# Optimization experiments

Hardware: AMD Instinct MI355X
Metric: run time of the kernel (lower is better)

Reference implementation:

```python
import jax, jax.numpy as jnp
import numpy as np

N_NODES = 100000
N_EDGES = 1600000
IN_DIM = 256
OUT_DIM = 128
SELF_LOOP_W = 2.0  # improved=True


def setup_inputs() -> dict:
    key = jax.random.key(0)
    ks = jax.random.split(key, 9)
    x = jax.random.normal(ks[0], (N_NODES, IN_DIM), dtype=jnp.float32)
    edge_index = jax.random.randint(ks[1], (2, N_EDGES), 0, N_NODES, dtype=jnp.int64)
    edge_weight = jax.random.uniform(ks[2], (N_EDGES,), dtype=jnp.float32)
    s1 = 1.0 / np.sqrt(IN_DIM)
    s2 = 1.0 / np.sqrt(OUT_DIM)
    W1 = jax.random.normal(ks[3], (IN_DIM, OUT_DIM), dtype=jnp.float32) * s1
    b1 = jnp.zeros((OUT_DIM,), dtype=jnp.float32)
    W_mu = jax.random.normal(ks[4], (OUT_DIM, OUT_DIM), dtype=jnp.float32) * s2
    b_mu = jnp.zeros((OUT_DIM,), dtype=jnp.float32)
    W_var = jax.random.normal(ks[5], (OUT_DIM, OUT_DIM), dtype=jnp.float32) * s2
    b_var = jnp.zeros((OUT_DIM,), dtype=jnp.float32)
    return {"x": x, "edge_index": edge_index, "edge_weight": edge_weight,
            "W1": W1, "b1": b1, "W_mu": W_mu, "b_mu": b_mu,
            "W_var": W_var, "b_var": b_var}


def _gcn_norm(edge_index, edge_weight, num_nodes):
    # add self loops with fill value 2.0 (improved=True), then symmetric norm
    loop = jnp.arange(num_nodes, dtype=edge_index.dtype)
    row = jnp.concatenate([edge_index[0], loop])
    col = jnp.concatenate([edge_index[1], loop])
    ew = jnp.concatenate([edge_weight,
                          jnp.full((num_nodes,), SELF_LOOP_W, dtype=edge_weight.dtype)])
    deg = jax.ops.segment_sum(ew, col, num_segments=num_nodes)
    dis = jnp.where(deg > 0, jax.lax.rsqrt(jnp.where(deg > 0, deg, 1.0)), 0.0)
    norm = dis[row] * ew * dis[col]
    return row, col, norm


def _gcn_conv(x, row, col, norm, W, b, num_nodes):
    xw = x @ W                      # [N, out]
    msg = xw[row] * norm[:, None]   # [E+N, out] per-edge messages
    out = jax.ops.segment_sum(msg, col, num_segments=num_nodes)
    return out + b


def reference(x, edge_index, edge_weight, W1, b1, W_mu, b_mu, W_var, b_var):
    n = x.shape[0]
    row, col, norm = _gcn_norm(edge_index, edge_weight, n)
    feat = jax.nn.relu(_gcn_conv(x, row, col, norm, W1, b1, n))
    mu = _gcn_conv(feat, row, col, norm, W_mu, b_mu, n)
    var = _gcn_conv(feat, row, col, norm, W_var, b_var, n)
    return (mu, var)
```

## Files before the change

### kernel.cpp

```cpp
#include <hip/hip_runtime.h>
#include <hip/hip_bf16.h>

#define CDIV(a,b) (((a)+(b)-1)/(b))

typedef __attribute__((ext_vector_type(8))) short short8;
typedef __attribute__((ext_vector_type(4))) float f32x4;

static __device__ inline short f2bf(float f) {
    union { __hip_bfloat16 h; short s; } u;
    u.h = __float2bfloat16(f);
    return u.s;
}
static __device__ inline ushort f2bfu(float f) { return (ushort)f2bf(f); }
static __device__ inline float bfu_lo(uint v) { return __uint_as_float(v << 16); }
static __device__ inline float bfu_hi(uint v) { return __uint_as_float(v & 0xffff0000u); }


__global__ __launch_bounds__(512) void k_init(unsigned long long* __restrict__ pack, int n,
                                              const float* __restrict__ W1,
                                              short* __restrict__ W1t,
                                              const float* __restrict__ Wmu,
                                              const float* __restrict__ Wvar,
                                              short* __restrict__ Wcat) {
    int i = blockIdx.x * 512 + threadIdx.x;
    if (i < n) pack[i] = 0ull;
    if (i < 128 * 256) {
        int k = i % 256, col = i / 256;
        W1t[i] = f2bf(W1[(size_t)k * 128 + col]);
    } else if (i < 2 * 128 * 256) {
        int j = i - 128 * 256;
        int k = j & 127, col = j >> 7;
        float v = (col < 128) ? Wmu[(size_t)k * 128 + col] : Wvar[(size_t)k * 128 + (col - 128)];
        Wcat[j] = f2bf(v);
    }
}


__global__ __launch_bounds__(512) void k_fat(const float* __restrict__ A,
                                             const short* __restrict__ Bt,
                                             ushort* __restrict__ C, int n, int nGB,
                                             const int* __restrict__ col,
                                             const float* __restrict__ ew,
                                             unsigned long long* __restrict__ pack,
                                             int* __restrict__ rank, int E) {
    const int K = 256, KH = 128;
    __shared__ short Blds[128 * KH];
    int t = threadIdx.x;

    if (blockIdx.x >= nGB) {
        int e = (blockIdx.x - nGB) * 512 + t;
        if (e < E) {
            int c = col[e];
            unsigned long long q = (unsigned long long)(ew[e] * 16777216.0f + 0.5f);
            unsigned long long old = atomicAdd(&pack[c], (1ull << 40) | q);
            rank[e] = (int)(old >> 40);
        }
        return;
    }

    int wave = t >> 6, lane = t & 63;
    int lg = lane >> 4, lr = lane & 15;
    long row_base = (long)blockIdx.x * 256 + wave * 32;

    long ra0 = row_base + lr;      if (ra0 > n - 1) ra0 = n - 1;
    long ra1 = row_base + 16 + lr; if (ra1 > n - 1) ra1 = n - 1;

    f32x4 acc[2][8];
    #pragma unroll
    for (int i = 0; i < 2; ++i)
        #pragma unroll
        for (int j = 0; j < 8; ++j) acc[i][j] = (f32x4){0.f, 0.f, 0.f, 0.f};

    const float* pa0 = A + ra0 * K + lg * 8;
    const float* pa1 = A + ra1 * K + lg * 8;

    #pragma unroll
    for (int p = 0; p < 2; ++p) {
        if (p) __syncthreads();
        const int CHK = KH / 8;
        for (int c = t; c < 128 * CHK; c += 512) {
            int colw = c / CHK;
            int kb  = (c % CHK) * 16;
            int dst = colw * (KH * 2) + (kb ^ ((colw & 7) << 4));
            *(float4*)((char*)Blds + dst) =
                *(const float4*)((const char*)Bt + (size_t)colw * (K * 2) + p * (KH * 2) + kb);
        }
        __syncthreads();

        for (int k0 = 0; k0 < KH; k0 += 32) {
            int kg = p * KH + k0;
            float4 x0 = *(const float4*)(pa0 + kg);
            float4 x1 = *(const float4*)(pa0 + kg + 4);
            float4 y0 = *(const float4*)(pa1 + kg);
            float4 y1 = *(const float4*)(pa1 + kg + 4);
            short8 a0, a1;
            a0[0]=f2bf(x0.x); a0[1]=f2bf(x0.y); a0[2]=f2bf(x0.z); a0[3]=f2bf(x0.w);
            a0[4]=f2bf(x1.x); a0[5]=f2bf(x1.y); a0[6]=f2bf(x1.z); a0[7]=f2bf(x1.w);
            a1[0]=f2bf(y0.x); a1[1]=f2bf(y0.y); a1[2]=f2bf(y0.z); a1[3]=f2bf(y0.w);
            a1[4]=f2bf(y1.x); a1[5]=f2bf(y1.y); a1[6]=f2bf(y1.z); a1[7]=f2bf(y1.w);

            int kb = (k0 + lg * 8) * 2;
            #pragma unroll
            for (int cb = 0; cb < 8; ++cb) {
                int colm = cb * 16 + lr;
                short8 b = *(short8*)((char*)Blds + colm * (KH * 2) + (kb ^ ((colm & 7) << 4)));
                acc[0][cb] = __builtin_amdgcn_mfma_f32_16x16x32_bf16(a0, b, acc[0][cb], 0, 0, 0);
                acc[1][cb] = __builtin_amdgcn_mfma_f32_16x16x32_bf16(a1, b, acc[1][cb], 0, 0, 0);
            }
        }
    }

    #pragma unroll
    for (int rf = 0; rf < 2; ++rf) {
        #pragma unroll
        for (int cb = 0; cb < 8; ++cb) {
            int colm = cb * 16 + lr;
            #pragma unroll
            for (int r = 0; r < 4; ++r) {
                long row = row_base + rf * 16 + lg * 4 + r;
                if (row < n) C[row * 128 + colm] = f2bfu(acc[rf][cb][r]);
            }
        }
    }
}


__global__ __launch_bounds__(256) void k_scan1(const unsigned long long* __restrict__ pack,
                                               float* __restrict__ dis,
                                               int* __restrict__ row_ptr,
                                               int* __restrict__ bsum, int n) {
    int t = threadIdx.x;
    int base = blockIdx.x * 1024 + t * 4;
    int v0 = 0, v1 = 0, v2 = 0, v3 = 0;
    #pragma unroll
    for (int j = 0; j < 4; ++j) {
        int idx = base + j;
        if (idx < n) {
            unsigned long long p = pack[idx];
            float deg = 2.0f + (float)(p & ((1ull << 40) - 1)) * (1.0f / 16777216.0f);
            dis[idx] = rsqrtf(deg);
            int c = (int)(p >> 40);
            if (j == 0) v0 = c; else if (j == 1) v1 = c; else if (j == 2) v2 = c; else v3 = c;
        }
    }
    int tsum = v0 + v1 + v2 + v3;
    int lane = t & 63, wv = t >> 6;
    int val = tsum;
    #pragma unroll
    for (int d = 1; d < 64; d <<= 1) {
        int u = __shfl_up(val, d, 64);
        if (lane >= d) val += u;
    }
    __shared__ int ws[4];
    if (lane == 63) ws[wv] = val;
    __syncthreads();
    int woff = 0;
    #pragma unroll
    for (int i = 0; i < 4; ++i) if (i < wv) woff += ws[i];
    int excl = woff + val - tsum;
    if (base + 0 < n) row_ptr[base + 0] = excl;  excl += v0;
    if (base + 1 < n) row_ptr[base + 1] = excl;  excl += v1;
    if (base + 2 < n) row_ptr[base + 2] = excl;  excl += v2;
    if (base + 3 < n) row_ptr[base + 3] = excl;
    if (t == 255) bsum[blockIdx.x] = woff + val;
}

__global__ __launch_bounds__(128) void k_scan2(int* bsum, int nb, int* row_ptr, int n, int E) {
    int t = threadIdx.x;
    int v = (t < nb) ? bsum[t] : 0;
    int lane = t & 63, wv = t >> 6;
    int val = v;
    #pragma unroll
    for (int d = 1; d < 64; d <<= 1) {
        int u = __shfl_up(val, d, 64);
        if (lane >= d) val += u;
    }
    __shared__ int ws[2];
    if (lane == 63) ws[wv] = val;
    __syncthreads();
    int woff = (wv == 1) ? ws[0] : 0;
    if (t < nb) bsum[t] = woff + val - v;
    if (t == 0) row_ptr[n] = E;
}

__global__ __launch_bounds__(256) void k_scan3(int* __restrict__ row_ptr,
                                               const int* __restrict__ bsum, int n) {
    int i = blockIdx.x * 256 + threadIdx.x;
    if (i < n) row_ptr[i] += bsum[i >> 10];
}

__global__ __launch_bounds__(512) void k_fill(const int* __restrict__ rowi,
                                              const int* __restrict__ coli,
                                              const float* __restrict__ ew,
                                              const int* __restrict__ rank,
                                              const float* __restrict__ dis,
                                              const int* __restrict__ row_ptr,
                                              int2* __restrict__ csr, int E) {
    int e = blockIdx.x * 512 + threadIdx.x;
    if (e < E) {
        int c = coli[e], r = rowi[e];
        int pos = row_ptr[c] + rank[e];
        csr[pos] = make_int2(r, __float_as_int(dis[r] * ew[e]));
    }
}


template<int OUTMODE>
__global__ __launch_bounds__(256) void k_agg(const uint2* __restrict__ src,
                                             const int* __restrict__ row_ptr,
                                             const int2* __restrict__ csr,
                                             const float* __restrict__ dis,
                                             const float* __restrict__ bias,
                                             uint2* __restrict__ dst, int n) {
    int wid = (blockIdx.x * 256 + threadIdx.x) >> 6;
    int lane = threadIdx.x & 63;
    int hb = lane >> 5, lc = lane & 31;
    if (wid >= n) return;
    int e0 = row_ptr[wid], e1 = row_ptr[wid + 1];

    float p00=0.f,p01=0.f,p02=0.f,p03=0.f;
    float p10=0.f,p11=0.f,p12=0.f,p13=0.f;
    float p20=0.f,p21=0.f,p22=0.f,p23=0.f;
    float p30=0.f,p31=0.f,p32=0.f,p33=0.f;

    int e = e0;
    for (; e + 7 < e1; e += 8) {
        int2 c0 = csr[e     + hb];
        int2 c1 = csr[e + 2 + hb];
        int2 c2 = csr[e + 4 + hb];
        int2 c3 = csr[e + 6 + hb];
        uint2 v0 = src[(size_t)c0.x * 32 + lc];
        uint2 v1 = src[(size_t)c1.x * 32 + lc];
        uint2 v2 = src[(size_t)c2.x * 32 + lc];
        uint2 v3 = src[(size_t)c3.x * 32 + lc];
        float w0 = __int_as_float(c0.y), w1 = __int_as_float(c1.y);
        float w2 = __int_as_float(c2.y), w3 = __int_as_float(c3.y);
        p00 += w0 * bfu_lo(v0.x); p01 += w0 * bfu_hi(v0.x);
        p02 += w0 * bfu_lo(v0.y); p03 += w0 * bfu_hi(v0.y);
        p10 += w1 * bfu_lo(v1.x); p11 += w1 * bfu_hi(v1.x);
        p12 += w1 * bfu_lo(v1.y); p13 += w1 * bfu_hi(v1.y);
        p20 += w2 * bfu_lo(v2.x); p21 += w2 * bfu_hi(v2.x);
        p22 += w2 * bfu_lo(v2.y); p23 += w2 * bfu_hi(v2.y);
        p30 += w3 * bfu_lo(v3.x); p31 += w3 * bfu_hi(v3.x);
        p32 += w3 * bfu_lo(v3.y); p33 += w3 * bfu_hi(v3.y);
    }
    for (; e + 1 < e1; e += 2) {
        int2 c = csr[e + hb];
        uint2 v = src[(size_t)c.x * 32 + lc];
        float w = __int_as_float(c.y);
        p00 += w * bfu_lo(v.x); p01 += w * bfu_hi(v.x);
        p02 += w * bfu_lo(v.y); p03 += w * bfu_hi(v.y);
    }
    if (e < e1 && hb == 0) {
        int2 c = csr[e];
        uint2 v = src[(size_t)c.x * 32 + lc];
        float w = __int_as_float(c.y);
        p10 += w * bfu_lo(v.x); p11 += w * bfu_hi(v.x);
        p12 += w * bfu_lo(v.y); p13 += w * bfu_hi(v.y);
    }

    float x0 = (p00 + p10) + (p20 + p30);
    float x1 = (p01 + p11) + (p21 + p31);
    float x2 = (p02 + p12) + (p22 + p32);
    float x3 = (p03 + p13) + (p23 + p33);
    x0 = x0 + __shfl_xor(x0, 32);
    x1 = x1 + __shfl_xor(x1, 32);
    x2 = x2 + __shfl_xor(x2, 32);
    x3 = x3 + __shfl_xor(x3, 32);

    float dc = dis[wid];
    uint2 sv = src[(size_t)wid * 32 + lc];
    float sw = 2.f * dc * dc;
    float o0 = dc * x0 + sw * bfu_lo(sv.x);
    float o1 = dc * x1 + sw * bfu_hi(sv.x);
    float o2 = dc * x2 + sw * bfu_lo(sv.y);
    float o3 = dc * x3 + sw * bfu_hi(sv.y);
    if constexpr (OUTMODE == 0) {
        float4 bv = *(const float4*)(bias + lc * 4);
        o0 += bv.x; o1 += bv.y; o2 += bv.z; o3 += bv.w;
        o0 = fmaxf(o0, 0.f); o1 = fmaxf(o1, 0.f);
        o2 = fmaxf(o2, 0.f); o3 = fmaxf(o3, 0.f);
    }
    if (hb == 0)
        dst[(size_t)wid * 32 + lc] =
            make_uint2((uint)f2bfu(o0) | ((uint)f2bfu(o1) << 16),
                       (uint)f2bfu(o2) | ((uint)f2bfu(o3) << 16));
}


__global__ __launch_bounds__(512) void k_gemm2(const short* __restrict__ A,
                                               const short* __restrict__ Bt,
                                               const float* __restrict__ bmu,
                                               const float* __restrict__ bvar,
                                               float* __restrict__ out,
                                               int n) {
    const int K = 128;
    __shared__ short Blds[256 * K];
    int t = threadIdx.x;

    const int CHK = K / 8;
    for (int c = t; c < 256 * CHK; c += 512) {
        int col = c / CHK;
        int kb  = (c % CHK) * 16;
        int dst = col * (K * 2) + (kb ^ ((col & 7) << 4));
        *(float4*)((char*)Blds + dst) =
            *(const float4*)((const char*)Bt + (size_t)col * (K * 2) + kb);
    }
    __syncthreads();

    int wave = t >> 6, lane = t & 63;
    int lg = lane >> 4, lr = lane & 15;
    int colbase = (wave & 1) * 128;
    long row_base = (long)blockIdx.x * 128 + (wave >> 1) * 32;

    long ra0 = row_base + lr;      if (ra0 > n - 1) ra0 = n - 1;
    long ra1 = row_base + 16 + lr; if (ra1 > n - 1) ra1 = n - 1;

    f32x4 acc[2][8];
    #pragma unroll
    for (int i = 0; i < 2; ++i)
        #pragma unroll
        for (int j = 0; j < 8; ++j) acc[i][j] = (f32x4){0.f, 0.f, 0.f, 0.f};

    const short* pa0 = A + ra0 * K + lg * 8;
    const short* pa1 = A + ra1 * K + lg * 8;

    #pragma unroll
    for (int k0 = 0; k0 < K; k0 += 32) {
        short8 a0 = *(const short8*)(pa0 + k0);
        short8 a1 = *(const short8*)(pa1 + k0);
        int kb = (k0 + lg * 8) * 2;
        #pragma unroll
        for (int cb = 0; cb < 8; ++cb) {
            int col = colbase + cb * 16 + lr;
            short8 b = *(short8*)((char*)Blds + col * (K * 2) + (kb ^ ((col & 7) << 4)));
            acc[0][cb] = __builtin_amdgcn_mfma_f32_16x16x32_bf16(a0, b, acc[0][cb], 0, 0, 0);
            acc[1][cb] = __builtin_amdgcn_mfma_f32_16x16x32_bf16(a1, b, acc[1][cb], 0, 0, 0);
        }
    }

    #pragma unroll
    for (int rf = 0; rf < 2; ++rf) {
        #pragma unroll
        for (int cb = 0; cb < 8; ++cb) {
            int colc = colbase + cb * 16 + lr;
            bool is_var = colc >= 128;
            int col = is_var ? colc - 128 : colc;
            float bv = is_var ? bvar[col] : bmu[col];
            size_t obase = is_var ? (size_t)n * 128 : 0;
            #pragma unroll
            for (int r = 0; r < 4; ++r) {
                long row = row_base + rf * 16 + lg * 4 + r;
                if (row < n)
                    __builtin_nontemporal_store(acc[rf][cb][r] + bv,
                                                &out[obase + (size_t)row * 128 + col]);
            }
        }
    }
}


extern "C" void kernel_launch(void* const* d_in, const int* in_sizes, int n_in,
                              void* d_out, int out_size, void* d_ws, size_t ws_size,
                              hipStream_t stream) {
    const float* x    = (const float*)d_in[0];
    const int*   ei   = (const int*)d_in[1];
    const float* ew   = (const float*)d_in[2];
    const float* W1   = (const float*)d_in[3];
    const float* b1   = (const float*)d_in[4];
    const float* Wmu  = (const float*)d_in[5];
    const float* bmu  = (const float*)d_in[6];
    const float* Wvar = (const float*)d_in[7];
    const float* bvar = (const float*)d_in[8];

    const int E = in_sizes[2];
    const int N = in_sizes[0] / 256;
    const int* rowi = ei;
    const int* coli = ei + E;

    char* base = (char*)d_ws;
    size_t off = 0;
    auto alloc = [&](size_t bytes) -> void* {
        void* p = base + off;
        off = (off + bytes + 511) & ~(size_t)511;
        return p;
    };
    unsigned long long* pack = (unsigned long long*)alloc((size_t)N * 8);
    float* dis     = (float*)alloc((size_t)N * 4);
    int*   row_ptr = (int*)  alloc((size_t)(N + 1) * 4);
    int*   rank    = (int*)  alloc((size_t)E * 4);
    int*   bsum    = (int*)  alloc(1024 * 4);
    int2*  csr     = (int2*) alloc((size_t)E * 8);
    uint*  xw      = (uint*) alloc((size_t)N * 64 * 4);
    uint*  feat    = (uint*) alloc((size_t)N * 64 * 4);
    short* W1t     = (short*)alloc((size_t)256 * 128 * 2);
    short* Wcat    = (short*)alloc((size_t)256 * 128 * 2);
    uint*  g       = xw;

    int nb   = CDIV(N, 1024);
    int nGB  = CDIV(N, 256);
    int nCB  = CDIV(E, 512);

    k_init<<<CDIV(N, 512), 512, 0, stream>>>(pack, N, W1, W1t, Wmu, Wvar, Wcat);

    k_fat<<<nGB + nCB, 512, 0, stream>>>(x, W1t, (ushort*)xw, N, nGB, coli, ew, pack, rank, E);

    k_scan1<<<nb, 256, 0, stream>>>(pack, dis, row_ptr, bsum, N);
    k_scan2<<<1, 128, 0, stream>>>(bsum, nb, row_ptr, N, E);
    k_scan3<<<CDIV(N, 256), 256, 0, stream>>>(row_ptr, bsum, N);
    k_fill <<<CDIV(E, 512), 512, 0, stream>>>(rowi, coli, ew, rank, dis, row_ptr, csr, E);

    k_agg<0><<<CDIV(N * 64, 256), 256, 0, stream>>>((const uint2*)xw, row_ptr, csr, dis, b1, (uint2*)feat, N);
    k_agg<1><<<CDIV(N * 64, 256), 256, 0, stream>>>((const uint2*)feat, row_ptr, csr, dis, nullptr, (uint2*)g, N);
    k_gemm2<<<CDIV(N, 128), 512, 0, stream>>>((const short*)g, Wcat, bmu, bvar, (float*)d_out, N);
}
```

Measured before the change: 307.1 us.

## Build CSR via two-level bucketed counting sort instead of global atomics

Replaces the global 64-bit atomicAdd degree/rank counting, which was fused into the GEMM launch, with a two-pass bucket sort. Edges are first histogrammed and scattered into 512-node buckets, then ranked and their weights summed with LDS atomics, and finally placed into the CSR. This is meant to remove contended global atomics and the random scatter. In exchange it adds many more kernel launches and extra passes over the edge arrays, and it no longer overlaps edge work with the first GEMM.

```diff
diff --git a/kernel.cpp b/kernel.cpp
--- a/kernel.cpp
+++ b/kernel.cpp
@@ -16,14 +16,12 @@
 static __device__ inline float bfu_hi(uint v) { return __uint_as_float(v & 0xffff0000u); }
 
 
-__global__ __launch_bounds__(512) void k_init(unsigned long long* __restrict__ pack, int n,
-                                              const float* __restrict__ W1,
+__global__ __launch_bounds__(512) void k_init(const float* __restrict__ W1,
                                               short* __restrict__ W1t,
                                               const float* __restrict__ Wmu,
                                               const float* __restrict__ Wvar,
                                               short* __restrict__ Wcat) {
     int i = blockIdx.x * 512 + threadIdx.x;
-    if (i < n) pack[i] = 0ull;
     if (i < 128 * 256) {
         int k = i % 256, col = i / 256;
         W1t[i] = f2bf(W1[(size_t)k * 128 + col]);
@@ -36,27 +34,150 @@
 }
 
 
-__global__ __launch_bounds__(512) void k_fat(const float* __restrict__ A,
-                                             const short* __restrict__ Bt,
-                                             ushort* __restrict__ C, int n, int nGB,
-                                             const int* __restrict__ col,
-                                             const float* __restrict__ ew,
-                                             unsigned long long* __restrict__ pack,
-                                             int* __restrict__ rank, int E) {
+__global__ __launch_bounds__(512) void k_bhist(const int* __restrict__ coli,
+                                               int* __restrict__ bhist,
+                                               int E, int chunk, int nbk) {
+    __shared__ int h[256];
+    int b = blockIdx.x, t = threadIdx.x, nblk = gridDim.x;
+    for (int i = t; i < nbk; i += 512) h[i] = 0;
+    __syncthreads();
+    int e0 = b * chunk, e1 = min(E, e0 + chunk);
+    for (int e = e0 + t; e < e1; e += 512)
+        atomicAdd(&h[coli[e] >> 9], 1);
+    __syncthreads();
+    for (int i = t; i < nbk; i += 512)
+        bhist[i * nblk + b] = h[i];
+}
+
+__global__ __launch_bounds__(256) void kscanA(const int* __restrict__ in,
+                                              int* __restrict__ out,
+                                              int* __restrict__ part, int n) {
+    int t = threadIdx.x;
+    int base = blockIdx.x * 1024 + t * 4;
+    int v0 = (base + 0 < n) ? in[base + 0] : 0;
+    int v1 = (base + 1 < n) ? in[base + 1] : 0;
+    int v2 = (base + 2 < n) ? in[base + 2] : 0;
+    int v3 = (base + 3 < n) ? in[base + 3] : 0;
+    int tsum = v0 + v1 + v2 + v3;
+    int lane = t & 63, wv = t >> 6;
+    int val = tsum;
+    #pragma unroll
+    for (int d = 1; d < 64; d <<= 1) {
+        int u = __shfl_up(val, d, 64);
+        if (lane >= d) val += u;
+    }
+    __shared__ int ws[4];
+    if (lane == 63) ws[wv] = val;
+    __syncthreads();
+    int woff = 0;
+    #pragma unroll
+    for (int i = 0; i < 4; ++i) if (i < wv) woff += ws[i];
+    int excl = woff + val - tsum;
+    if (base + 0 < n) out[base + 0] = excl;  excl += v0;
+    if (base + 1 < n) out[base + 1] = excl;  excl += v1;
+    if (base + 2 < n) out[base + 2] = excl;  excl += v2;
+    if (base + 3 < n) out[base + 3] = excl;
+    if (t == 255) part[blockIdx.x] = woff + val;
+}
+
+__global__ __launch_bounds__(128) void kscanB(int* part, int nb, int* tailp, int tailv) {
+    int t = threadIdx.x;
+    int v = (t < nb) ? part[t] : 0;
+    int lane = t & 63, wv = t >> 6;
+    int val = v;
+    #pragma unroll
+    for (int d = 1; d < 64; d <<= 1) {
+        int u = __shfl_up(val, d, 64);
+        if (lane >= d) val += u;
+    }
+    __shared__ int ws[2];
+    if (lane == 63) ws[wv] = val;
+    __syncthreads();
+    int woff = (wv == 1) ? ws[0] : 0;
+    if (t < nb) part[t] = woff + val - v;
+    if (t == 0 && tailp) *tailp = tailv;
+}
+
+__global__ __launch_bounds__(256) void kscanC(int* __restrict__ out,
+                                              const int* __restrict__ part, int n) {
+    int i = blockIdx.x * 256 + threadIdx.x;
+    if (i < n) out[i] += part[i >> 10];
+}
+
+__global__ __launch_bounds__(512) void k_bucket(const int* __restrict__ rowi,
+                                                const int* __restrict__ coli,
+                                                const float* __restrict__ ew,
+                                                const int* __restrict__ excl,
+                                                int* __restrict__ bcol,
+                                                int2* __restrict__ bre,
+                                                int E, int chunk, int nbk) {
+    __shared__ int cur[256];
+    int b = blockIdx.x, t = threadIdx.x, nblk = gridDim.x;
+    for (int i = t; i < nbk; i += 512) cur[i] = 0;
+    __syncthreads();
+    int e0 = b * chunk, e1 = min(E, e0 + chunk);
+    for (int e = e0 + t; e < e1; e += 512) {
+        int c = coli[e];
+        int bk = c >> 9;
+        int pos = excl[bk * nblk + b] + atomicAdd(&cur[bk], 1);
+        bcol[pos] = c;
+        bre[pos]  = make_int2(rowi[e], __float_as_int(ew[e]));
+    }
+}
+
+__global__ __launch_bounds__(512) void k_fine(const int* __restrict__ bcol,
+                                              const int2* __restrict__ bre,
+                                              const int* __restrict__ excl,
+                                              int* __restrict__ rank,
+                                              int* __restrict__ gcnt,
+                                              int* __restrict__ gews,
+                                              int E, int nblk, int n) {
+    __shared__ int cnt[512], ews[512];
+    int bk = blockIdx.x, t = threadIdx.x;
+    cnt[t] = 0; ews[t] = 0;
+    __syncthreads();
+    int s0 = excl[bk * nblk];
+    int s1 = (bk + 1 < gridDim.x) ? excl[(bk + 1) * nblk] : E;
+    for (int p = s0 + t; p < s1; p += 512) {
+        int cl = bcol[p] & 511;
+        rank[p] = atomicAdd(&cnt[cl], 1);
+        int q = (int)(__int_as_float(bre[p].y) * 16777216.0f + 0.5f);
+        atomicAdd(&ews[cl], q);
+    }
+    __syncthreads();
+    int c = bk * 512 + t;
+    if (c < n) { gcnt[c] = cnt[t]; gews[c] = ews[t]; }
+}
+
+__global__ __launch_bounds__(256) void k_dis(const int* __restrict__ gews,
+                                             float* __restrict__ dis, int n) {
+    int i = blockIdx.x * 256 + threadIdx.x;
+    if (i < n)
+        dis[i] = rsqrtf(2.0f + (float)gews[i] * (1.0f / 16777216.0f));
+}
+
+__global__ __launch_bounds__(512) void k_place(const int* __restrict__ bcol,
+                                               const int2* __restrict__ bre,
+                                               const int* __restrict__ rank,
+                                               const int* __restrict__ row_ptr,
+                                               const float* __restrict__ dis,
+                                               int2* __restrict__ csr, int E) {
+    int p = blockIdx.x * 512 + threadIdx.x;
+    if (p < E) {
+        int c = bcol[p];
+        int2 re = bre[p];
+        csr[row_ptr[c] + rank[p]] =
+            make_int2(re.x, __float_as_int(dis[re.x] * __int_as_float(re.y)));
+    }
+}
+
+
+__global__ __launch_bounds__(512) void k_gemm1(const float* __restrict__ A,
+                                               const short* __restrict__ Bt,
+                                               ushort* __restrict__ C, int n) {
     const int K = 256, KH = 128;
     __shared__ short Blds[128 * KH];
     int t = threadIdx.x;
-
-    if (blockIdx.x >= nGB) {
-        int e = (blockIdx.x - nGB) * 512 + t;
-        if (e < E) {
-            int c = col[e];
-            unsigned long long q = (unsigned long long)(ew[e] * 16777216.0f + 0.5f);
-            unsigned long long old = atomicAdd(&pack[c], (1ull << 40) | q);
-            rank[e] = (int)(old >> 40);
-        }
-        return;
-    }
 
     int wave = t >> 6, lane = t & 63;
     int lg = lane >> 4, lr = lane & 15;
@@ -103,9 +224,9 @@
             #pragma unroll
             for (int cb = 0; cb < 8; ++cb) {
                 int colm = cb * 16 + lr;
-                short8 b = *(short8*)((char*)Blds + colm * (KH * 2) + (kb ^ ((colm & 7) << 4)));
-                acc[0][cb] = __builtin_amdgcn_mfma_f32_16x16x32_bf16(a0, b, acc[0][cb], 0, 0, 0);
-                acc[1][cb] = __builtin_amdgcn_mfma_f32_16x16x32_bf16(a1, b, acc[1][cb], 0, 0, 0);
+                short8 bfr = *(short8*)((char*)Blds + colm * (KH * 2) + (kb ^ ((colm & 7) << 4)));
+                acc[0][cb] = __builtin_amdgcn_mfma_f32_16x16x32_bf16(a0, bfr, acc[0][cb], 0, 0, 0);
+                acc[1][cb] = __builtin_amdgcn_mfma_f32_16x16x32_bf16(a1, bfr, acc[1][cb], 0, 0, 0);
             }
         }
     }
@@ -121,86 +242,6 @@
                 if (row < n) C[row * 128 + colm] = f2bfu(acc[rf][cb][r]);
             }
         }
-    }
-}
-
-
-__global__ __launch_bounds__(256) void k_scan1(const unsigned long long* __restrict__ pack,
-                                               float* __restrict__ dis,
-                                               int* __restrict__ row_ptr,
-                                               int* __restrict__ bsum, int n) {
-    int t = threadIdx.x;
-    int base = blockIdx.x * 1024 + t * 4;
-    int v0 = 0, v1 = 0, v2 = 0, v3 = 0;
-    #pragma unroll
-    for (int j = 0; j < 4; ++j) {
-        int idx = base + j;
-        if (idx < n) {
-            unsigned long long p = pack[idx];
-            float deg = 2.0f + (float)(p & ((1ull << 40) - 1)) * (1.0f / 16777216.0f);
-            dis[idx] = rsqrtf(deg);
-            int c = (int)(p >> 40);
-            if (j == 0) v0 = c; else if (j == 1) v1 = c; else if (j == 2) v2 = c; else v3 = c;
-        }
-    }
-    int tsum = v0 + v1 + v2 + v3;
-    int lane = t & 63, wv = t >> 6;
-    int val = tsum;
-    #pragma unroll
-    for (int d = 1; d < 64; d <<= 1) {
-        int u = __shfl_up(val, d, 64);
-        if (lane >= d) val += u;
-    }
-    __shared__ int ws[4];
-    if (lane == 63) ws[wv] = val;
-    __syncthreads();
-    int woff = 0;
-    #pragma unroll
-    for (int i = 0; i < 4; ++i) if (i < wv) woff += ws[i];
-    int excl = woff + val - tsum;
-    if (base + 0 < n) row_ptr[base + 0] = excl;  excl += v0;
-    if (base + 1 < n) row_ptr[base + 1] = excl;  excl += v1;
-    if (base + 2 < n) row_ptr[base + 2] = excl;  excl += v2;
-    if (base + 3 < n) row_ptr[base + 3] = excl;
-    if (t == 255) bsum[blockIdx.x] = woff + val;
-}
-
-__global__ __launch_bounds__(128) void k_scan2(int* bsum, int nb, int* row_ptr, int n, int E) {
-    int t = threadIdx.x;
-    int v = (t < nb) ? bsum[t] : 0;
-    int lane = t & 63, wv = t >> 6;
-    int val = v;
-    #pragma unroll
-    for (int d = 1; d < 64; d <<= 1) {
-        int u = __shfl_up(val, d, 64);
-        if (lane >= d) val += u;
-    }
-    __shared__ int ws[2];
-    if (lane == 63) ws[wv] = val;
-    __syncthreads();
-    int woff = (wv == 1) ? ws[0] : 0;
-    if (t < nb) bsum[t] = woff + val - v;
-    if (t == 0) row_ptr[n] = E;
-}
-
-__global__ __launch_bounds__(256) void k_scan3(int* __restrict__ row_ptr,
-                                               const int* __restrict__ bsum, int n) {
-    int i = blockIdx.x * 256 + threadIdx.x;
-    if (i < n) row_ptr[i] += bsum[i >> 10];
-}
-
-__global__ __launch_bounds__(512) void k_fill(const int* __restrict__ rowi,
-                                              const int* __restrict__ coli,
-                                              const float* __restrict__ ew,
-                                              const int* __restrict__ rank,
-                                              const float* __restrict__ dis,
-                                              const int* __restrict__ row_ptr,
-                                              int2* __restrict__ csr, int E) {
-    int e = blockIdx.x * 512 + threadIdx.x;
-    if (e < E) {
-        int c = coli[e], r = rowi[e];
-        int pos = row_ptr[c] + rank[e];
-        csr[pos] = make_int2(r, __float_as_int(dis[r] * ew[e]));
     }
 }
 
@@ -385,11 +426,21 @@
         off = (off + bytes + 511) & ~(size_t)511;
         return p;
     };
-    unsigned long long* pack = (unsigned long long*)alloc((size_t)N * 8);
+    const int NBLK = 256;
+    const int nbk  = CDIV(N, 512);
+    const int chunk = CDIV(E, NBLK);
+    const int nh   = nbk * NBLK;
+
+    int*   bhist   = (int*)  alloc((size_t)nh * 4);
+    int*   excl    = (int*)  alloc((size_t)nh * 4);
+    int*   part    = (int*)  alloc(256 * 4);
+    int*   bcol    = (int*)  alloc((size_t)E * 4);
+    int2*  bre     = (int2*) alloc((size_t)E * 8);
+    int*   rank    = (int*)  alloc((size_t)E * 4);
+    int*   gcnt    = (int*)  alloc((size_t)N * 4);
+    int*   gews    = (int*)  alloc((size_t)N * 4);
+    int*   row_ptr = (int*)  alloc((size_t)(N + 1) * 4);
     float* dis     = (float*)alloc((size_t)N * 4);
-    int*   row_ptr = (int*)  alloc((size_t)(N + 1) * 4);
-    int*   rank    = (int*)  alloc((size_t)E * 4);
-    int*   bsum    = (int*)  alloc(1024 * 4);
     int2*  csr     = (int2*) alloc((size_t)E * 8);
     uint*  xw      = (uint*) alloc((size_t)N * 64 * 4);
     uint*  feat    = (uint*) alloc((size_t)N * 64 * 4);
@@ -397,18 +448,21 @@
     short* Wcat    = (short*)alloc((size_t)256 * 128 * 2);
     uint*  g       = xw;
 
-    int nb   = CDIV(N, 1024);
-    int nGB  = CDIV(N, 256);
-    int nCB  = CDIV(E, 512);
-
-    k_init<<<CDIV(N, 512), 512, 0, stream>>>(pack, N, W1, W1t, Wmu, Wvar, Wcat);
-
-    k_fat<<<nGB + nCB, 512, 0, stream>>>(x, W1t, (ushort*)xw, N, nGB, coli, ew, pack, rank, E);
-
-    k_scan1<<<nb, 256, 0, stream>>>(pack, dis, row_ptr, bsum, N);
-    k_scan2<<<1, 128, 0, stream>>>(bsum, nb, row_ptr, N, E);
-    k_scan3<<<CDIV(N, 256), 256, 0, stream>>>(row_ptr, bsum, N);
-    k_fill <<<CDIV(E, 512), 512, 0, stream>>>(rowi, coli, ew, rank, dis, row_ptr, csr, E);
+    k_init<<<CDIV(2 * 128 * 256, 512), 512, 0, stream>>>(W1, W1t, Wmu, Wvar, Wcat);
+
+    k_gemm1<<<CDIV(N, 256), 512, 0, stream>>>(x, W1t, (ushort*)xw, N);
+
+    k_bhist<<<NBLK, 512, 0, stream>>>(coli, bhist, E, chunk, nbk);
+    kscanA<<<CDIV(nh, 1024), 256, 0, stream>>>(bhist, excl, part, nh);
+    kscanB<<<1, 128, 0, stream>>>(part, CDIV(nh, 1024), nullptr, 0);
+    kscanC<<<CDIV(nh, 256), 256, 0, stream>>>(excl, part, nh);
+    k_bucket<<<NBLK, 512, 0, stream>>>(rowi, coli, ew, excl, bcol, bre, E, chunk, nbk);
+    k_fine<<<nbk, 512, 0, stream>>>(bcol, bre, excl, rank, gcnt, gews, E, NBLK, N);
+    kscanA<<<CDIV(N, 1024), 256, 0, stream>>>(gcnt, row_ptr, part, N);
+    kscanB<<<1, 128, 0, stream>>>(part, CDIV(N, 1024), &row_ptr[N], E);
+    kscanC<<<CDIV(N, 256), 256, 0, stream>>>(row_ptr, part, N);
+    k_dis<<<CDIV(N, 256), 256, 0, stream>>>(gews, dis, N);
+    k_place<<<CDIV(E, 512), 512, 0, stream>>>(bcol, bre, rank, row_ptr, dis, csr, E);
 
     k_agg<0><<<CDIV(N * 64, 256), 256, 0, stream>>>((const uint2*)xw, row_ptr, csr, dis, b1, (uint2*)feat, N);
     k_agg<1><<<CDIV(N * 64, 256), 256, 0, stream>>>((const uint2*)feat, row_ptr, csr, dis, nullptr, (uint2*)g, N);
```

New measurement: 286.6 us. -6.7%, faster.
